# Performance work log

Hardware: AMD Instinct MI355X
Metric: run time of the kernel (lower is better)

The kernel has to match this reference:

```python
import jax, jax.numpy as jnp
import numpy as np
import math

B, T, C = 2, 2048, 1024
N_HEAD = 16
HEAD_DIM = C // N_HEAD


def setup_inputs() -> dict:
    key = jax.random.key(0)
    k1, k2, k3 = jax.random.split(key, 3)
    x = jax.random.normal(k1, (B, T, C), dtype=jnp.float32)
    # causal mask: positions where mask == 0 get -inf
    mask = jnp.tril(jnp.ones((T, T), dtype=bool))[None, None, :, :]
    W_attn = jax.random.normal(k2, (C, 3 * C), dtype=jnp.float32) * (1.0 / math.sqrt(C))
    b_attn = jnp.zeros((3 * C,), dtype=jnp.float32)
    W_proj = jax.random.normal(k3, (C, C), dtype=jnp.float32) * (1.0 / math.sqrt(C))
    b_proj = jnp.zeros((C,), dtype=jnp.float32)
    return {"x": x, "mask": mask, "W_attn": W_attn, "b_attn": b_attn,
            "W_proj": W_proj, "b_proj": b_proj}


def reference(x, mask, W_attn, b_attn, W_proj, b_proj):
    Bx, Tx, Cx = x.shape
    qkv = x @ W_attn + b_attn                      # [B,T,3C]
    q, k, v = jnp.split(qkv, 3, axis=2)
    # [B,T,C] -> [B,H,T,D]
    q = q.reshape(Bx, Tx, N_HEAD, HEAD_DIM).transpose(0, 2, 1, 3)
    k = k.reshape(Bx, Tx, N_HEAD, HEAD_DIM).transpose(0, 2, 1, 3)
    v = v.reshape(Bx, Tx, N_HEAD, HEAD_DIM).transpose(0, 2, 1, 3)
    scale = 1.0 / math.sqrt(HEAD_DIM)
    att = jnp.einsum('bhqd,bhkd->bhqk', q, k) * scale   # [B,H,T,T]
    att = jnp.where(mask, att, -jnp.inf)
    att = jax.nn.softmax(att, axis=-1)
    y = jnp.einsum('bhqk,bhkd->bhqd', att, v)            # [B,H,T,D]
    y = y.transpose(0, 2, 1, 3).reshape(Bx, Tx, Cx)      # [B,T,C]
    return y @ W_proj + b_proj
```

## Files before the change

kernel.cpp:

```cpp
#include <hip/hip_runtime.h>
#include <hip/hip_bf16.h>
#include <cstdint>

typedef unsigned short u16;
typedef unsigned int u32;
typedef unsigned long long u64;
using f32x4 = __attribute__((ext_vector_type(4))) float;
using s16x8 = __attribute__((ext_vector_type(8))) short;
using u32x4 = __attribute__((ext_vector_type(4))) u32;

#define NB 2
#define NT 2048
#define NC 1024
#define NH 16
#define HD 64

__device__ __forceinline__ u16 f2b(float f) {
    unsigned u = __float_as_uint(f);
    unsigned r = (u + 0x7FFFu + ((u >> 16) & 1u)) >> 16;
    return (u16)r;
}

__device__ __forceinline__ u32 cvtpk(float a, float b) {
    u32 r;
    asm("v_cvt_pk_bf16_f32 %0, %1, %2" : "=v"(r) : "v"(a), "v"(b));
    return r;
}
__device__ __forceinline__ void swap32(u32& a, u32& b) {
    asm("v_permlane32_swap_b32 %0, %1" : "+v"(a), "+v"(b));
}
__device__ __forceinline__ void swap16(u32& a, u32& b) {
    asm("v_permlane16_swap_b32 %0, %1" : "+v"(a), "+v"(b));
}

__device__ __forceinline__ void gl_lds16(const void* g, const void* l) {
    __builtin_amdgcn_global_load_lds(
        (const __attribute__((address_space(1))) unsigned int*)g,
        (__attribute__((address_space(3))) unsigned int*)l, 16, 0, 0);
}

__global__ __launch_bounds__(256) void prep(const float* __restrict__ x,
                                            u16* __restrict__ xb,
                                            const float* __restrict__ Wa,
                                            u16* __restrict__ WaT,
                                            const float* __restrict__ Wp,
                                            u16* __restrict__ WpT) {
    __shared__ u16 s[64][65];
    const int bid = blockIdx.x;
    const int t = threadIdx.x;

    if (bid < 4096) {
        int i = bid * 256 + t;
        float4 v = ((const float4*)x)[i];
        u64 pack = (u64)f2b(v.x) | ((u64)f2b(v.y) << 16) |
                   ((u64)f2b(v.z) << 32) | ((u64)f2b(v.w) << 48);
        ((u64*)xb)[i] = pack;
        return;
    }

    const float* W; u16* Wt; int K, N, n0, k0;
    if (bid < 4096 + 768) {
        int q = bid - 4096;
        W = Wa; Wt = WaT; K = 1024; N = 3072;
        n0 = (q % 48) * 64; k0 = (q / 48) * 64;
    } else {
        int q = bid - 4096 - 768;
        W = Wp; Wt = WpT; K = 1024; N = 1024;
        n0 = (q % 16) * 64; k0 = (q / 16) * 64;
    }

    const int tr = t >> 4, tc4 = (t & 15) * 4;
#pragma unroll
    for (int i = 0; i < 4; i++) {
        int r = tr + i * 16;
        float4 v = *(const float4*)&W[(size_t)(k0 + r) * N + n0 + tc4];
        s[r][tc4 + 0] = f2b(v.x);
        s[r][tc4 + 1] = f2b(v.y);
        s[r][tc4 + 2] = f2b(v.z);
        s[r][tc4 + 3] = f2b(v.w);
    }
    __syncthreads();
#pragma unroll
    for (int i = 0; i < 4; i++) {
        int nl = tr + i * 16;
        u64 pack = (u64)s[tc4 + 0][nl] | ((u64)s[tc4 + 1][nl] << 16) |
                   ((u64)s[tc4 + 2][nl] << 32) | ((u64)s[tc4 + 3][nl] << 48);
        *(u64*)&Wt[(size_t)(n0 + nl) * K + k0 + tc4] = pack;
    }
}

template <int OUT_BF16>
__global__ __launch_bounds__(256) void gemm_bt(const u16* __restrict__ A,
                                               const u16* __restrict__ Bt,
                                               const float* __restrict__ bias,
                                               void* __restrict__ Cout,
                                               int M, int N, int K) {
    __shared__ u16 As[2][128 * 32];
    __shared__ u16 Bs[2][128 * 32];
    const int tid = threadIdx.x;
    const int lane = tid & 63, w = tid >> 6;
    const int nx = gridDim.x;
    const int f = blockIdx.y * nx + blockIdx.x;
    const int qq = (nx * gridDim.y) >> 3;
    const int nid = (f & 7) * qq + (f >> 3);
    const int m0 = (nid / nx) * 128, n0 = (nid % nx) * 128;
    const int wm = w >> 1, wn = w & 1;
    f32x4 acc[4][4] = {};

    const int srow = 32 * w + (lane >> 2);
    const int scol = (((lane & 3) ^ ((lane >> 2) & 3)) * 8);
    const u16* aP0 = &A[(size_t)(m0 + srow) * K + scol];
    const u16* aP1 = aP0 + (size_t)16 * K;
    const u16* bP0 = &Bt[(size_t)(n0 + srow) * K + scol];
    const u16* bP1 = bP0 + (size_t)16 * K;

    auto STAGE = [&](int t) {
        const int buf = t & 1;
        const int k0 = t * 32;
        gl_lds16(aP0 + k0, &As[buf][w * 1024 + lane * 8]);
        gl_lds16(aP1 + k0, &As[buf][w * 1024 + 512 + lane * 8]);
        gl_lds16(bP0 + k0, &Bs[buf][w * 1024 + lane * 8]);
        gl_lds16(bP1 + k0, &Bs[buf][w * 1024 + 512 + lane * 8]);
    };

    const int rchunk = (((lane >> 4) ^ (lane & 3)) * 8);

    const int nt = K >> 5;
    STAGE(0);
    for (int t = 0; t < nt; ++t) {
        asm volatile("s_waitcnt vmcnt(0)" ::: "memory");
        __builtin_amdgcn_s_barrier();
        if (t + 1 < nt) STAGE(t + 1);

        const u16* Asb = As[t & 1];
        const u16* Bsb = Bs[t & 1];
        s16x8 af[4], bf[4];
#pragma unroll
        for (int mt = 0; mt < 4; mt++)
            af[mt] = *(const s16x8*)&Asb[(wm * 64 + mt * 16 + (lane & 15)) * 32 + rchunk];
#pragma unroll
        for (int nt2 = 0; nt2 < 4; nt2++)
            bf[nt2] = *(const s16x8*)&Bsb[(wn * 64 + nt2 * 16 + (lane & 15)) * 32 + rchunk];
        __builtin_amdgcn_s_setprio(1);
#pragma unroll
        for (int mt = 0; mt < 4; mt++)
#pragma unroll
            for (int nt2 = 0; nt2 < 4; nt2++)
                acc[mt][nt2] = __builtin_amdgcn_mfma_f32_16x16x32_bf16(af[mt], bf[nt2], acc[mt][nt2], 0, 0, 0);
        __builtin_amdgcn_s_setprio(0);
    }

#pragma unroll
    for (int mt = 0; mt < 4; mt++) {
        int row = m0 + wm * 64 + mt * 16 + (lane >> 4) * 4;
#pragma unroll
        for (int nt2 = 0; nt2 < 4; nt2++) {
            int col = n0 + wn * 64 + nt2 * 16 + (lane & 15);
            float bs = bias[col];
#pragma unroll
            for (int r = 0; r < 4; r++) {
                float v = acc[mt][nt2][r] + bs;
                if (OUT_BF16)
                    ((u16*)Cout)[(size_t)(row + r) * N + col] = f2b(v);
                else
                    ((float*)Cout)[(size_t)(row + r) * N + col] = v;
            }
        }
    }
}

__global__ __launch_bounds__(256) void gemm_bt_n64(const u16* __restrict__ A,
                                                   const u16* __restrict__ Bt,
                                                   const float* __restrict__ bias,
                                                   float* __restrict__ Cout,
                                                   int M, int N, int K) {
    __shared__ u16 As[2][128 * 32];
    __shared__ u16 Bs[2][64 * 32];
    const int tid = threadIdx.x;
    const int lane = tid & 63, w = tid >> 6;
    const int nx = gridDim.x;
    const int f = blockIdx.y * nx + blockIdx.x;
    const int qq = (nx * gridDim.y) >> 3;
    const int nid = (f & 7) * qq + (f >> 3);
    const int m0 = (nid / nx) * 128, n0 = (nid % nx) * 64;
    f32x4 acc[2][4] = {};

    const int srow = 32 * w + (lane >> 2);
    const int srowB = 16 * w + (lane >> 2);
    const int scol = (((lane & 3) ^ ((lane >> 2) & 3)) * 8);
    const u16* aP0 = &A[(size_t)(m0 + srow) * K + scol];
    const u16* aP1 = aP0 + (size_t)16 * K;
    const u16* bP0 = &Bt[(size_t)(n0 + srowB) * K + scol];

    auto STAGE = [&](int t) {
        const int buf = t & 1;
        const int k0 = t * 32;
        gl_lds16(aP0 + k0, &As[buf][w * 1024 + lane * 8]);
        gl_lds16(aP1 + k0, &As[buf][w * 1024 + 512 + lane * 8]);
        gl_lds16(bP0 + k0, &Bs[buf][w * 512 + lane * 8]);
    };

    const int rchunk = (((lane >> 4) ^ (lane & 3)) * 8);

    const int nt = K >> 5;
    STAGE(0);
    for (int t = 0; t < nt; ++t) {
        asm volatile("s_waitcnt vmcnt(0)" ::: "memory");
        __builtin_amdgcn_s_barrier();
        if (t + 1 < nt) STAGE(t + 1);

        const u16* Asb = As[t & 1];
        const u16* Bsb = Bs[t & 1];
        s16x8 af[2], bf[4];
#pragma unroll
        for (int mt = 0; mt < 2; mt++)
            af[mt] = *(const s16x8*)&Asb[(w * 32 + mt * 16 + (lane & 15)) * 32 + rchunk];
#pragma unroll
        for (int nt2 = 0; nt2 < 4; nt2++)
            bf[nt2] = *(const s16x8*)&Bsb[(nt2 * 16 + (lane & 15)) * 32 + rchunk];
        __builtin_amdgcn_s_setprio(1);
#pragma unroll
        for (int mt = 0; mt < 2; mt++)
#pragma unroll
            for (int nt2 = 0; nt2 < 4; nt2++)
                acc[mt][nt2] = __builtin_amdgcn_mfma_f32_16x16x32_bf16(af[mt], bf[nt2], acc[mt][nt2], 0, 0, 0);
        __builtin_amdgcn_s_setprio(0);
    }

#pragma unroll
    for (int mt = 0; mt < 2; mt++) {
        int row = m0 + w * 32 + mt * 16 + (lane >> 4) * 4;
#pragma unroll
        for (int nt2 = 0; nt2 < 4; nt2++) {
            int col = n0 + nt2 * 16 + (lane & 15);
            float bs = bias[col];
#pragma unroll
            for (int r = 0; r < 4; r++)
                Cout[(size_t)(row + r) * N + col] = acc[mt][nt2][r] + bs;
        }
    }
}

__global__ __launch_bounds__(256) void v_transpose(const u16* __restrict__ qkv,
                                                   u16* __restrict__ Vt) {
    __shared__ u16 s[64][65];
    const int t0 = blockIdx.x * 64;
    const int b = blockIdx.y >> 4, h = blockIdx.y & 15;
    const int t = threadIdx.x;
    const int tr = t >> 4, tc4 = (t & 15) * 4;
    const u16* src = qkv + (size_t)b * NT * (3 * NC) + 2 * NC + h * HD;
#pragma unroll
    for (int i = 0; i < 4; i++) {
        int r = tr + i * 16;
        u64 v = *(const u64*)&src[(size_t)(t0 + r) * (3 * NC) + tc4];
        s[r][tc4 + 0] = (u16)v;
        s[r][tc4 + 1] = (u16)(v >> 16);
        s[r][tc4 + 2] = (u16)(v >> 32);
        s[r][tc4 + 3] = (u16)(v >> 48);
    }
    __syncthreads();
    u16* dstb = Vt + (size_t)(b * NH + h) * HD * NT;
#pragma unroll
    for (int i = 0; i < 4; i++) {
        int d = tr + i * 16;
        u64 pack = (u64)s[tc4 + 0][d] | ((u64)s[tc4 + 1][d] << 16) |
                   ((u64)s[tc4 + 2][d] << 32) | ((u64)s[tc4 + 3][d] << 48);
        *(u64*)&dstb[(size_t)d * NT + t0 + tc4] = pack;
    }
}

__global__ __launch_bounds__(512) void attn_kernel(const u16* __restrict__ qkv,
                                                   const u16* __restrict__ Vt,
                                                   u16* __restrict__ yb) {
    __shared__ __align__(16) u16 Kb[2][2][64 * 64];
    __shared__ __align__(16) u16 Vb[2][2][64 * 64];

    const int l = threadIdx.x & 63;
    const int q16 = l & 15, g = l >> 4;
    const int wv = threadIdx.x >> 6;
    const int rg = wv & 3, hf = wv >> 2;
    const int i0 = blockIdx.x;
    const int xcd = i0 & 7, idx = i0 >> 3;
    const int hh = xcd * 4 + (idx >> 4);
    const int pr = idx & 15;
    const int b = hh >> 4, h = hh & 15;

    const u16* qkvb = qkv + (size_t)b * NT * (3 * NC);

    const int srow = l >> 3;
    const int sc8 = (l & 7) ^ (srow & 7);
    const u16* kSrc0 = qkvb + NC + h * HD + (size_t)(8 * rg + srow) * (3 * NC) + sc8 * 8;
    const u16* kSrc1 = kSrc0 + (size_t)32 * (3 * NC);
    const u16* vSrc0 = Vt + ((size_t)(b * NH + h) * HD + 8 * rg + srow) * NT + sc8 * 8;
    const u16* vSrc1 = vSrc0 + (size_t)32 * NT;
    const size_t kStep = (size_t)64 * (3 * NC);

    const float sc2 = 0.125f * 1.44269504088896340736f;
    const float SHIFT = 5.0f * 1.44269504088896340736f;
    const int sw = q16 & 7;

    u32 kfo[4][2], vfo[2][4];
#pragma unroll
    for (int ii = 0; ii < 4; ii++)
#pragma unroll
        for (int kc = 0; kc < 2; kc++)
            kfo[ii][kc] = (u32)(((16 * ii + q16) * 64 + ((4 * kc + g) ^ sw) * 8) * 2);
#pragma unroll
    for (int ks = 0; ks < 2; ks++)
#pragma unroll
        for (int dt = 0; dt < 4; dt++)
            vfo[ks][dt] = (u32)(((16 * dt + q16) * 64 + ((4 * ks + g) ^ sw) * 8) * 2);

#pragma unroll 1
    for (int sc = 0; sc < 2; ++sc) {
        const int cc = (sc == 0) ? (31 - pr) : pr;
        const int nt = cc + 1;
        const int h0 = (nt + 1) >> 1;
        const int base = hf ? h0 : 0;
        const int myN = hf ? (nt - h0) : h0;
        const int qw = cc * 64 + 16 * rg;

        s16x8 qf[2];
#pragma unroll
        for (int kc = 0; kc < 2; kc++)
            qf[kc] = *(const s16x8*)(qkvb + (size_t)(qw + q16) * (3 * NC) + h * HD + kc * 32 + g * 8);

        f32x4 yacc[4] = {};
        float lsum = 0.f;

        const u16* kP0 = kSrc0 + (size_t)base * kStep;
        const u16* kP1 = kSrc1 + (size_t)base * kStep;
        const u16* vP0 = vSrc0 + base * 64;
        const u16* vP1 = vSrc1 + base * 64;

        auto STAGE = [&](int buf) {
            gl_lds16(kP0, &Kb[hf][buf][rg * 512 + l * 8]);
            gl_lds16(kP1, &Kb[hf][buf][2048 + rg * 512 + l * 8]);
            gl_lds16(vP0, &Vb[hf][buf][rg * 512 + l * 8]);
            gl_lds16(vP1, &Vb[hf][buf][2048 + rg * 512 + l * 8]);
            kP0 += kStep; kP1 += kStep; vP0 += 64; vP1 += 64;
        };

        if (myN > 0) STAGE(base & 1);
        for (int u = 0; u < h0; ++u) {
            const int t = base + u;
            const bool act = (u < myN);
            asm volatile("s_waitcnt vmcnt(0)" ::: "memory");
            __builtin_amdgcn_s_barrier();
            if (u + 1 < myN) STAGE((t + 1) & 1);

            if (act) {
                const char* Kc = (const char*)&Kb[hf][t & 1][0];
                const char* Vc = (const char*)&Vb[hf][t & 1][0];

                s16x8 kf[4][2];
#pragma unroll
                for (int ii = 0; ii < 4; ii++)
#pragma unroll
                    for (int kc = 0; kc < 2; kc++)
                        kf[ii][kc] = *(const s16x8*)(Kc + kfo[ii][kc]);

                s16x8 vf0[4];
#pragma unroll
                for (int dt = 0; dt < 4; dt++)
                    vf0[dt] = *(const s16x8*)(Vc + vfo[0][dt]);

                f32x4 sacc[4] = {};
                __builtin_amdgcn_s_setprio(1);
#pragma unroll
                for (int ii = 0; ii < 4; ii++)
#pragma unroll
                    for (int kc = 0; kc < 2; kc++)
                        sacc[ii] = __builtin_amdgcn_mfma_f32_16x16x32_bf16(kf[ii][kc], qf[kc], sacc[ii], 0, 0, 0);
                __builtin_amdgcn_s_setprio(0);

                if (t == cc) {
                    const int kv0 = t * 64;
#pragma unroll
                    for (int ii = 0; ii < 4; ii++)
#pragma unroll
                        for (int r = 0; r < 4; r++)
                            if (kv0 + 16 * ii + 4 * g + r > qw + q16) sacc[ii][r] = -1e30f;
                }

                float p[4][4];
                float ps = 0.f;
#pragma unroll
                for (int ii = 0; ii < 4; ii++)
#pragma unroll
                    for (int r = 0; r < 4; r++) {
                        p[ii][r] = exp2f(fmaf(sacc[ii][r], sc2, -SHIFT));
                        ps += p[ii][r];
                    }
                lsum += ps;

                s16x8 pfrag[2];
#pragma unroll
                for (int ks = 0; ks < 2; ks++) {
                    u32 C0 = cvtpk(p[2 * ks][0], p[2 * ks][1]);
                    u32 C1 = cvtpk(p[2 * ks][2], p[2 * ks][3]);
                    u32 D0 = cvtpk(p[2 * ks + 1][0], p[2 * ks + 1][1]);
                    u32 D1 = cvtpk(p[2 * ks + 1][2], p[2 * ks + 1][3]);
                    swap32(C0, D0); swap16(C0, D0);
                    swap32(C1, D1); swap16(C1, D1);
                    u32x4 fr;
                    fr[0] = C0; fr[1] = C1; fr[2] = D0; fr[3] = D1;
                    pfrag[ks] = __builtin_bit_cast(s16x8, fr);
                }

                s16x8 vf1[4];
#pragma unroll
                for (int dt = 0; dt < 4; dt++)
                    vf1[dt] = *(const s16x8*)(Vc + vfo[1][dt]);

                __builtin_amdgcn_s_setprio(1);
#pragma unroll
                for (int dt = 0; dt < 4; dt++)
                    yacc[dt] = __builtin_amdgcn_mfma_f32_16x16x32_bf16(vf0[dt], pfrag[0], yacc[dt], 0, 0, 0);
#pragma unroll
                for (int dt = 0; dt < 4; dt++)
                    yacc[dt] = __builtin_amdgcn_mfma_f32_16x16x32_bf16(vf1[dt], pfrag[1], yacc[dt], 0, 0, 0);
                __builtin_amdgcn_s_setprio(0);
            }
        }
        __builtin_amdgcn_s_barrier();

        float* mY = (float*)&Kb[1][0][0];
        float* mL = (float*)&Vb[1][0][0];
        if (hf == 1) {
#pragma unroll
            for (int dt = 0; dt < 4; dt++)
#pragma unroll
                for (int r = 0; r < 4; r++)
                    mY[(rg * 16 + dt * 4 + r) * 64 + l] = yacc[dt][r];
            mL[rg * 64 + l] = lsum;
        }
        __syncthreads();
        if (hf == 0) {
#pragma unroll
            for (int dt = 0; dt < 4; dt++)
#pragma unroll
                for (int r = 0; r < 4; r++)
                    yacc[dt][r] += mY[(rg * 16 + dt * 4 + r) * 64 + l];
            lsum += mL[rg * 64 + l];
            lsum += __shfl_xor(lsum, 16);
            lsum += __shfl_xor(lsum, 32);
            float inv = 1.f / lsum;
            size_t rowoff = ((size_t)(b * NT + qw + q16)) * NC + h * HD;
#pragma unroll
            for (int dt = 0; dt < 4; dt++) {
                u32 lo = cvtpk(yacc[dt][0] * inv, yacc[dt][1] * inv);
                u32 hi = cvtpk(yacc[dt][2] * inv, yacc[dt][3] * inv);
                u64 pk = (u64)lo | ((u64)hi << 32);
                *(u64*)(yb + rowoff + 16 * dt + 4 * g) = pk;
            }
        }
        __syncthreads();
    }
}

extern "C" void kernel_launch(void* const* d_in, const int* in_sizes, int n_in,
                              void* d_out, int out_size, void* d_ws, size_t ws_size,
                              hipStream_t stream) {
    const float* x  = (const float*)d_in[0];
    const float* Wa = (const float*)d_in[2];
    const float* ba = (const float*)d_in[3];
    const float* Wp = (const float*)d_in[4];
    const float* bp = (const float*)d_in[5];
    float* out = (float*)d_out;

    char* ws = (char*)d_ws;
    u16* xb  = (u16*)(ws);
    u16* WaT = (u16*)(ws + (8ull << 20));
    u16* WpT = (u16*)(ws + (14ull << 20));
    u16* qkv = (u16*)(ws + (16ull << 20));
    u16* yb  = (u16*)(ws + (40ull << 20));
    u16* Vtb = (u16*)(ws + (48ull << 20));

    const int M = NB * NT;

    prep<<<dim3(4096 + 768 + 256), 256, 0, stream>>>(x, xb, Wa, WaT, Wp, WpT);

    gemm_bt<1><<<dim3(3 * NC / 128, M / 128), 256, 0, stream>>>(xb, WaT, ba, qkv, M, 3 * NC, NC);

    v_transpose<<<dim3(NT / 64, NB * NH), 256, 0, stream>>>(qkv, Vtb);

    attn_kernel<<<dim3(NB * NH * 16), 512, 0, stream>>>(qkv, Vtb, yb);

    gemm_bt_n64<<<dim3(NC / 64, M / 128), 256, 0, stream>>>(yb, WpT, bp, out, M, NC, NC);
}
```

Baseline: 114.4 us.

## Software-pipeline attention loop so QK^T of next tile overlaps softmax/PV

Restructures the inner KV loop so that the score MFMAs for tile t are issued before the softmax and PV MFMAs of tile t-1. The previous tile's scores and V fragments are carried in registers, and a final drain step handles the last tile together with the causal diagonal mask. LDS offset tables are replaced by two base offsets plus constant strides. The aim is to overlap exp and pack work with matrix-core work. It raises register pressure, which could lower occupancy or cause spills.

```diff
diff --git a/kernel.cpp b/kernel.cpp
--- a/kernel.cpp
+++ b/kernel.cpp
@@ -299,17 +299,8 @@
     const float SHIFT = 5.0f * 1.44269504088896340736f;
     const int sw = q16 & 7;
 
-    u32 kfo[4][2], vfo[2][4];
-#pragma unroll
-    for (int ii = 0; ii < 4; ii++)
-#pragma unroll
-        for (int kc = 0; kc < 2; kc++)
-            kfo[ii][kc] = (u32)(((16 * ii + q16) * 64 + ((4 * kc + g) ^ sw) * 8) * 2);
-#pragma unroll
-    for (int ks = 0; ks < 2; ks++)
-#pragma unroll
-        for (int dt = 0; dt < 4; dt++)
-            vfo[ks][dt] = (u32)(((16 * dt + q16) * 64 + ((4 * ks + g) ^ sw) * 8) * 2);
+    const u32 kfB0 = (u32)((q16 * 64 + ((g) ^ sw) * 8) * 2);
+    const u32 kfB1 = (u32)((q16 * 64 + ((4 + g) ^ sw) * 8) * 2);
 
 #pragma unroll 1
     for (int sc = 0; sc < 2; ++sc) {
@@ -341,6 +332,47 @@
             kP0 += kStep; kP1 += kStep; vP0 += 64; vP1 += 64;
         };
 
+        f32x4 saccP[4];
+        s16x8 vfp[2][4];
+
+        auto SOFTPV = [&](bool diag) {
+            if (diag) {
+                const int kv0 = cc * 64;
+#pragma unroll
+                for (int ii = 0; ii < 4; ii++)
+#pragma unroll
+                    for (int r = 0; r < 4; r++)
+                        if (kv0 + 16 * ii + 4 * g + r > qw + q16) saccP[ii][r] = -1e30f;
+            }
+            float ps = 0.f;
+#pragma unroll
+            for (int ks = 0; ks < 2; ks++) {
+                float p[2][4];
+#pragma unroll
+                for (int jj = 0; jj < 2; jj++)
+#pragma unroll
+                    for (int r = 0; r < 4; r++) {
+                        p[jj][r] = exp2f(fmaf(saccP[2 * ks + jj][r], sc2, -SHIFT));
+                        ps += p[jj][r];
+                    }
+                u32 C0 = cvtpk(p[0][0], p[0][1]);
+                u32 C1 = cvtpk(p[0][2], p[0][3]);
+                u32 D0 = cvtpk(p[1][0], p[1][1]);
+                u32 D1 = cvtpk(p[1][2], p[1][3]);
+                swap32(C0, D0); swap16(C0, D0);
+                swap32(C1, D1); swap16(C1, D1);
+                u32x4 fr;
+                fr[0] = C0; fr[1] = C1; fr[2] = D0; fr[3] = D1;
+                s16x8 pf = __builtin_bit_cast(s16x8, fr);
+                __builtin_amdgcn_s_setprio(1);
+#pragma unroll
+                for (int dt = 0; dt < 4; dt++)
+                    yacc[dt] = __builtin_amdgcn_mfma_f32_16x16x32_bf16(vfp[ks][dt], pf, yacc[dt], 0, 0, 0);
+                __builtin_amdgcn_s_setprio(0);
+            }
+            lsum += ps;
+        };
+
         if (myN > 0) STAGE(base & 1);
         for (int u = 0; u < h0; ++u) {
             const int t = base + u;
@@ -353,76 +385,46 @@
                 const char* Kc = (const char*)&Kb[hf][t & 1][0];
                 const char* Vc = (const char*)&Vb[hf][t & 1][0];
 
-                s16x8 kf[4][2];
-#pragma unroll
-                for (int ii = 0; ii < 4; ii++)
-#pragma unroll
-                    for (int kc = 0; kc < 2; kc++)
-                        kf[ii][kc] = *(const s16x8*)(Kc + kfo[ii][kc]);
-
-                s16x8 vf0[4];
-#pragma unroll
-                for (int dt = 0; dt < 4; dt++)
-                    vf0[dt] = *(const s16x8*)(Vc + vfo[0][dt]);
-
-                f32x4 sacc[4] = {};
-                __builtin_amdgcn_s_setprio(1);
-#pragma unroll
-                for (int ii = 0; ii < 4; ii++)
-#pragma unroll
-                    for (int kc = 0; kc < 2; kc++)
-                        sacc[ii] = __builtin_amdgcn_mfma_f32_16x16x32_bf16(kf[ii][kc], qf[kc], sacc[ii], 0, 0, 0);
-                __builtin_amdgcn_s_setprio(0);
-
-                if (t == cc) {
-                    const int kv0 = t * 64;
-#pragma unroll
-                    for (int ii = 0; ii < 4; ii++)
-#pragma unroll
-                        for (int r = 0; r < 4; r++)
-                            if (kv0 + 16 * ii + 4 * g + r > qw + q16) sacc[ii][r] = -1e30f;
+                f32x4 sN0 = {0.f,0.f,0.f,0.f}, sN1 = {0.f,0.f,0.f,0.f};
+                f32x4 sN2 = {0.f,0.f,0.f,0.f}, sN3 = {0.f,0.f,0.f,0.f};
+                {
+                    s16x8 a0 = *(const s16x8*)(Kc + kfB0);
+                    s16x8 a1 = *(const s16x8*)(Kc + kfB1);
+                    s16x8 b0 = *(const s16x8*)(Kc + kfB0 + 2048);
+                    s16x8 b1 = *(const s16x8*)(Kc + kfB1 + 2048);
+                    __builtin_amdgcn_s_setprio(1);
+                    sN0 = __builtin_amdgcn_mfma_f32_16x16x32_bf16(a0, qf[0], sN0, 0, 0, 0);
+                    sN0 = __builtin_amdgcn_mfma_f32_16x16x32_bf16(a1, qf[1], sN0, 0, 0, 0);
+                    sN1 = __builtin_amdgcn_mfma_f32_16x16x32_bf16(b0, qf[0], sN1, 0, 0, 0);
+                    sN1 = __builtin_amdgcn_mfma_f32_16x16x32_bf16(b1, qf[1], sN1, 0, 0, 0);
+                    __builtin_amdgcn_s_setprio(0);
                 }
-
-                float p[4][4];
-                float ps = 0.f;
-#pragma unroll
-                for (int ii = 0; ii < 4; ii++)
-#pragma unroll
-                    for (int r = 0; r < 4; r++) {
-                        p[ii][r] = exp2f(fmaf(sacc[ii][r], sc2, -SHIFT));
-                        ps += p[ii][r];
-                    }
-                lsum += ps;
-
-                s16x8 pfrag[2];
-#pragma unroll
-                for (int ks = 0; ks < 2; ks++) {
-                    u32 C0 = cvtpk(p[2 * ks][0], p[2 * ks][1]);
-                    u32 C1 = cvtpk(p[2 * ks][2], p[2 * ks][3]);
-                    u32 D0 = cvtpk(p[2 * ks + 1][0], p[2 * ks + 1][1]);
-                    u32 D1 = cvtpk(p[2 * ks + 1][2], p[2 * ks + 1][3]);
-                    swap32(C0, D0); swap16(C0, D0);
-                    swap32(C1, D1); swap16(C1, D1);
-                    u32x4 fr;
-                    fr[0] = C0; fr[1] = C1; fr[2] = D0; fr[3] = D1;
-                    pfrag[ks] = __builtin_bit_cast(s16x8, fr);
+                {
+                    s16x8 a0 = *(const s16x8*)(Kc + kfB0 + 4096);
+                    s16x8 a1 = *(const s16x8*)(Kc + kfB1 + 4096);
+                    s16x8 b0 = *(const s16x8*)(Kc + kfB0 + 6144);
+                    s16x8 b1 = *(const s16x8*)(Kc + kfB1 + 6144);
+                    __builtin_amdgcn_s_setprio(1);
+                    sN2 = __builtin_amdgcn_mfma_f32_16x16x32_bf16(a0, qf[0], sN2, 0, 0, 0);
+                    sN2 = __builtin_amdgcn_mfma_f32_16x16x32_bf16(a1, qf[1], sN2, 0, 0, 0);
+                    sN3 = __builtin_amdgcn_mfma_f32_16x16x32_bf16(b0, qf[0], sN3, 0, 0, 0);
+                    sN3 = __builtin_amdgcn_mfma_f32_16x16x32_bf16(b1, qf[1], sN3, 0, 0, 0);
+                    __builtin_amdgcn_s_setprio(0);
                 }
 
-                s16x8 vf1[4];
-#pragma unroll
-                for (int dt = 0; dt < 4; dt++)
-                    vf1[dt] = *(const s16x8*)(Vc + vfo[1][dt]);
-
-                __builtin_amdgcn_s_setprio(1);
-#pragma unroll
-                for (int dt = 0; dt < 4; dt++)
-                    yacc[dt] = __builtin_amdgcn_mfma_f32_16x16x32_bf16(vf0[dt], pfrag[0], yacc[dt], 0, 0, 0);
-#pragma unroll
-                for (int dt = 0; dt < 4; dt++)
-                    yacc[dt] = __builtin_amdgcn_mfma_f32_16x16x32_bf16(vf1[dt], pfrag[1], yacc[dt], 0, 0, 0);
-                __builtin_amdgcn_s_setprio(0);
+                if (u > 0) SOFTPV(false);
+
+#pragma unroll
+                for (int dt = 0; dt < 4; dt++) {
+                    vfp[0][dt] = *(const s16x8*)(Vc + kfB0 + dt * 2048);
+                    vfp[1][dt] = *(const s16x8*)(Vc + kfB1 + dt * 2048);
+                }
+
+                saccP[0] = sN0; saccP[1] = sN1; saccP[2] = sN2; saccP[3] = sN3;
             }
         }
+        if (myN > 0) SOFTPV(base + myN - 1 == cc);
+
         __builtin_amdgcn_s_barrier();
 
         float* mY = (float*)&Kb[1][0][0];
```

After: 121.1 us. 5.8% more time.
